# Kernel tuning notes

Measured on AMD Instinct MI355X. Metric: run time of the kernel, lower is better.

The kernel has to match this reference:

```python
import jax, jax.numpy as jnp
import numpy as np

TEMPERATURE = 0.5
NEG_INF = -1e9  # used to mask self-similarity diagonal before logsumexp


def setup_inputs() -> dict:
    key = jax.random.key(0)
    k1, k2 = jax.random.split(key)
    N, Z = 4096, 128
    z1 = jax.random.normal(k1, (N, Z), dtype=jnp.float32)
    z2 = jax.random.normal(k2, (N, Z), dtype=jnp.float32)
    return {"z1": z1, "z2": z2}


def reference(z1, z2):
    # NT-Xent (SimCLR) loss. Faithful to:
    #   sim = cosine_similarity over all pairs of concat([z1, z2])
    #   positives = sim diagonals at offsets +-N; negatives = all off-(self)diag entries
    #   cross_entropy with the positive as class 0  ->  -pos/T + logsumexp(all non-self sims / T)
    N = z1.shape[0]
    reps = jnp.concatenate([z1, z2], axis=0)                      # [2N, Z]
    # row-normalize once; cosine sim matrix is then a single GEMM
    norms = jnp.linalg.norm(reps, axis=-1, keepdims=True)
    # torch cosine_similarity clamps norms by eps=1e-8
    nreps = reps / jnp.maximum(norms, 1e-8)
    sim = nreps @ nreps.T                                          # [2N, 2N]
    # positives: sim[i, i+N] for i<N and sim[i, i-N] for i>=N
    l_pos = jnp.diagonal(sim, offset=N)                            # [N]
    r_pos = jnp.diagonal(sim, offset=-N)                           # [N]
    positives = jnp.concatenate([l_pos, r_pos])                    # [2N]
    # logsumexp over all entries except the self-similarity diagonal.
    # (The positive entry stays in the denominator exactly once, matching
    #  concat([positive, negatives]) in the original.)
    two_n = 2 * N
    self_mask = jnp.eye(two_n, dtype=bool)
    logits = jnp.where(self_mask, NEG_INF, sim / TEMPERATURE)      # [2N, 2N]
    lse = jax.nn.logsumexp(logits, axis=1)                         # [2N]
    per_row = lse - positives / TEMPERATURE                        # CE with label 0
    return jnp.sum(per_row) / two_n
```

## Files before the change

kernel.cpp:

```cpp
#include <hip/hip_runtime.h>
#include <hip/hip_bf16.h>


#define N_PAIRS 4096
#define ZDIM    128
#define NROWS   8192
#define QS 1.6986437717f

typedef __bf16 bf16x8 __attribute__((ext_vector_type(8)));
typedef float  floatx4 __attribute__((ext_vector_type(4)));

__global__ __launch_bounds__(256) void k_normalize(
    const float* __restrict__ z1, const float* __restrict__ z2,
    __hip_bfloat16* __restrict__ pack, float* __restrict__ pos,
    float* __restrict__ denom)
{
    const int zi = blockIdx.x * 256 + threadIdx.x;
    if (zi < NROWS) denom[zi] = 0.0f;

    const int w = threadIdx.x >> 6;
    const int lane = threadIdx.x & 63;
    const int p = blockIdx.x * 4 + w;
    const float2 a = ((const float2*)(z1 + (size_t)p * ZDIM))[lane];
    const float2 b = ((const float2*)(z2 + (size_t)p * ZDIM))[lane];
    float s1 = a.x * a.x + a.y * a.y;
    float s2 = b.x * b.x + b.y * b.y;
    float d  = a.x * b.x + a.y * b.y;
    #pragma unroll
    for (int off = 1; off < 64; off <<= 1) {
        s1 += __shfl_xor(s1, off, 64);
        s2 += __shfl_xor(s2, off, 64);
        d  += __shfl_xor(d,  off, 64);
    }
    const float n1 = fmaxf(sqrtf(s1), 1e-8f);
    const float n2 = fmaxf(sqrtf(s2), 1e-8f);
    const float i1 = 1.0f / n1, i2 = 1.0f / n2;
    const float q1 = i1 * QS, q2 = i2 * QS;
    float2 na; na.x = a.x * q1; na.y = a.y * q1;
    float2 nb; nb.x = b.x * q2; nb.y = b.y * q2;

    const int ks = lane >> 4;
    const int qq = (lane >> 2) & 3;
    const int jj = (lane & 3) * 2;
    const int r1 = p, r2 = p + N_PAIRS;
    const size_t i1e = ((size_t)((r1 >> 4) * 4 + ks)) * 512 + qq * 128 + (r1 & 15) * 8 + jj;
    const size_t i2e = ((size_t)((r2 >> 4) * 4 + ks)) * 512 + qq * 128 + (r2 & 15) * 8 + jj;
    *(__hip_bfloat162*)(pack + i1e) = __float22bfloat162_rn(na);
    *(__hip_bfloat162*)(pack + i2e) = __float22bfloat162_rn(nb);
    if (lane == 0) pos[p] = d * i1 * i2;
}

__global__ __launch_bounds__(256) void k_simsum(
    const __hip_bfloat16* __restrict__ pack, float* __restrict__ denom)
{
    const int tid  = threadIdx.x;
    const int lane = tid & 63;
    const int w    = tid >> 6;
    const int rt   = blockIdx.x >> 4;
    const int cs   = blockIdx.x & 15;
    const int q    = lane >> 4;
    const int l16  = lane & 15;

    const int rowb = rt * 128 + w * 32;
    const __hip_bfloat16* Abase =
        pack + ((size_t)(rowb >> 4) * 4) * 512 + lane * 8;
    bf16x8 afrag[2][4];
    #pragma unroll
    for (int mt = 0; mt < 2; ++mt)
        #pragma unroll
        for (int ks = 0; ks < 4; ++ks)
            afrag[mt][ks] = *(const bf16x8*)(Abase + mt * 2048 + ks * 512);

    float rowsum[2][4];
    #pragma unroll
    for (int mt = 0; mt < 2; ++mt)
        #pragma unroll
        for (int r = 0; r < 4; ++r) rowsum[mt][r] = 0.0f;

    for (int it = 0; it < 8; ++it) {
        floatx4 acc[2][4];
        #pragma unroll
        for (int mt = 0; mt < 2; ++mt)
            #pragma unroll
            for (int nt = 0; nt < 4; ++nt) {
                acc[mt][nt].x = 0.f; acc[mt][nt].y = 0.f;
                acc[mt][nt].z = 0.f; acc[mt][nt].w = 0.f;
            }
        const int colb = cs * 512 + it * 64;
        const __hip_bfloat16* Bbase =
            pack + ((size_t)(colb >> 4) * 4) * 512 + lane * 8;
        bf16x8 bfrag[4][4];
        #pragma unroll
        for (int nt = 0; nt < 4; ++nt)
            #pragma unroll
            for (int ks = 0; ks < 4; ++ks)
                bfrag[nt][ks] = *(const bf16x8*)(Bbase + nt * 2048 + ks * 512);
        #pragma unroll
        for (int ks = 0; ks < 4; ++ks)
            #pragma unroll
            for (int mt = 0; mt < 2; ++mt)
                #pragma unroll
                for (int nt = 0; nt < 4; ++nt)
                    acc[mt][nt] = __builtin_amdgcn_mfma_f32_16x16x32_bf16(
                        afrag[mt][ks], bfrag[nt][ks], acc[mt][nt], 0, 0, 0);
        #pragma unroll
        for (int mt = 0; mt < 2; ++mt) {
            const int rowtb = rowb + mt * 16;
            #pragma unroll
            for (int nt = 0; nt < 4; ++nt) {
                const int coltb = colb + nt * 16;
                if (rowtb == coltb) {
                    #pragma unroll
                    for (int r = 0; r < 4; ++r) {
                        const float e = __builtin_amdgcn_exp2f(acc[mt][nt][r]);
                        rowsum[mt][r] += (l16 == q * 4 + r) ? 0.0f : e;
                    }
                } else {
                    #pragma unroll
                    for (int r = 0; r < 4; ++r)
                        rowsum[mt][r] += __builtin_amdgcn_exp2f(acc[mt][nt][r]);
                }
            }
        }
    }

    #pragma unroll
    for (int mt = 0; mt < 2; ++mt)
        #pragma unroll
        for (int r = 0; r < 4; ++r) {
            float s = rowsum[mt][r];
            s += __shfl_xor(s, 1, 64);
            s += __shfl_xor(s, 2, 64);
            s += __shfl_xor(s, 4, 64);
            s += __shfl_xor(s, 8, 64);
            rowsum[mt][r] = s;
        }
    if (l16 == 0) {
        #pragma unroll
        for (int mt = 0; mt < 2; ++mt)
            #pragma unroll
            for (int r = 0; r < 4; ++r) {
                const int grow = rowb + mt * 16 + q * 4 + r;
                atomicAdd(&denom[grow], rowsum[mt][r]);
            }
    }
}

__global__ __launch_bounds__(1024) void k_finish(
    const float* __restrict__ denom, const float* __restrict__ pos,
    float* __restrict__ out)
{
    __shared__ float red[1024];
    const int t = threadIdx.x;
    float s = 0.0f;
    for (int i = t; i < NROWS; i += 1024) s += __logf(denom[i]);
    float p = 0.0f;
    for (int i = t; i < N_PAIRS; i += 1024) p += pos[i];
    red[t] = s - 4.0f * p;
    __syncthreads();
    for (int off = 512; off > 0; off >>= 1) {
        if (t < off) red[t] += red[t + off];
        __syncthreads();
    }
    if (t == 0) out[0] = red[0] / (float)NROWS;
}

extern "C" void kernel_launch(void* const* d_in, const int* in_sizes, int n_in,
                              void* d_out, int out_size, void* d_ws, size_t ws_size,
                              hipStream_t stream) {
    const float* z1 = (const float*)d_in[0];
    const float* z2 = (const float*)d_in[1];
    float* out = (float*)d_out;

    char* ws = (char*)d_ws;
    __hip_bfloat16* pack = (__hip_bfloat16*)ws;
    float* denom = (float*)(ws + (size_t)NROWS * ZDIM * 2);
    float* pos   = denom + NROWS;

    k_normalize<<<N_PAIRS / 4, 256, 0, stream>>>(z1, z2, pack, pos, denom);
    k_simsum<<<1024, 256, 0, stream>>>(pack, denom);
    k_finish<<<1, 1024, 0, stream>>>(denom, pos, out);
}
```

Before: 87.64 us.

## Exploit similarity matrix symmetry by computing only upper-triangular tiles

```diff
diff --git a/kernel.cpp b/kernel.cpp
--- a/kernel.cpp
+++ b/kernel.cpp
@@ -53,11 +53,14 @@
 __global__ __launch_bounds__(256) void k_simsum(
     const __hip_bfloat16* __restrict__ pack, float* __restrict__ denom)
 {
+    const int rt = blockIdx.x;
+    const int ct = blockIdx.y;
+    if (ct < rt) return;
+    const bool diag = (rt == ct);
+
     const int tid  = threadIdx.x;
     const int lane = tid & 63;
     const int w    = tid >> 6;
-    const int rt   = blockIdx.x >> 4;
-    const int cs   = blockIdx.x & 15;
     const int q    = lane >> 4;
     const int l16  = lane & 15;
 
@@ -72,12 +75,14 @@
             afrag[mt][ks] = *(const bf16x8*)(Abase + mt * 2048 + ks * 512);
 
     float rowsum[2][4];
-    #pragma unroll
-    for (int mt = 0; mt < 2; ++mt)
-        #pragma unroll
-        for (int r = 0; r < 4; ++r) rowsum[mt][r] = 0.0f;
-
-    for (int it = 0; it < 8; ++it) {
+    float colsum[2][4];
+    #pragma unroll
+    for (int a = 0; a < 2; ++a)
+        #pragma unroll
+        for (int b = 0; b < 4; ++b) { rowsum[a][b] = 0.0f; colsum[a][b] = 0.0f; }
+
+    #pragma unroll
+    for (int it = 0; it < 2; ++it) {
         floatx4 acc[2][4];
         #pragma unroll
         for (int mt = 0; mt < 2; ++mt)
@@ -86,7 +91,7 @@
                 acc[mt][nt].x = 0.f; acc[mt][nt].y = 0.f;
                 acc[mt][nt].z = 0.f; acc[mt][nt].w = 0.f;
             }
-        const int colb = cs * 512 + it * 64;
+        const int colb = ct * 128 + it * 64;
         const __hip_bfloat16* Bbase =
             pack + ((size_t)(colb >> 4) * 4) * 512 + lane * 8;
         bf16x8 bfrag[4][4];
@@ -103,24 +108,38 @@
                 for (int nt = 0; nt < 4; ++nt)
                     acc[mt][nt] = __builtin_amdgcn_mfma_f32_16x16x32_bf16(
                         afrag[mt][ks], bfrag[nt][ks], acc[mt][nt], 0, 0, 0);
-        #pragma unroll
-        for (int mt = 0; mt < 2; ++mt) {
-            const int rowtb = rowb + mt * 16;
-            #pragma unroll
-            for (int nt = 0; nt < 4; ++nt) {
-                const int coltb = colb + nt * 16;
-                if (rowtb == coltb) {
+
+        if (diag) {
+            #pragma unroll
+            for (int mt = 0; mt < 2; ++mt) {
+                const int rowtb = w * 32 + mt * 16;
+                #pragma unroll
+                for (int nt = 0; nt < 4; ++nt) {
+                    const int coltb = it * 64 + nt * 16;
+                    if (rowtb == coltb) {
+                        #pragma unroll
+                        for (int r = 0; r < 4; ++r) {
+                            const float e = __builtin_amdgcn_exp2f(acc[mt][nt][r]);
+                            rowsum[mt][r] += (l16 == q * 4 + r) ? 0.0f : e;
+                        }
+                    } else {
+                        #pragma unroll
+                        for (int r = 0; r < 4; ++r)
+                            rowsum[mt][r] += __builtin_amdgcn_exp2f(acc[mt][nt][r]);
+                    }
+                }
+            }
+        } else {
+            #pragma unroll
+            for (int mt = 0; mt < 2; ++mt)
+                #pragma unroll
+                for (int nt = 0; nt < 4; ++nt)
                     #pragma unroll
                     for (int r = 0; r < 4; ++r) {
                         const float e = __builtin_amdgcn_exp2f(acc[mt][nt][r]);
-                        rowsum[mt][r] += (l16 == q * 4 + r) ? 0.0f : e;
+                        rowsum[mt][r] += e;
+                        colsum[it][nt] += e;
                     }
-                } else {
-                    #pragma unroll
-                    for (int r = 0; r < 4; ++r)
-                        rowsum[mt][r] += __builtin_amdgcn_exp2f(acc[mt][nt][r]);
-                }
-            }
         }
     }
 
@@ -144,25 +163,42 @@
                 atomicAdd(&denom[grow], rowsum[mt][r]);
             }
     }
+    if (!diag) {
+        #pragma unroll
+        for (int it = 0; it < 2; ++it)
+            #pragma unroll
+            for (int nt = 0; nt < 4; ++nt) {
+                float s = colsum[it][nt];
+                s += __shfl_xor(s, 16, 64);
+                s += __shfl_xor(s, 32, 64);
+                if (q == 0)
+                    atomicAdd(&denom[ct * 128 + it * 64 + nt * 16 + l16], s);
+            }
+    }
 }
 
 __global__ __launch_bounds__(1024) void k_finish(
     const float* __restrict__ denom, const float* __restrict__ pos,
     float* __restrict__ out)
 {
-    __shared__ float red[1024];
+    __shared__ float red[16];
     const int t = threadIdx.x;
+    const int lane = t & 63, wv = t >> 6;
     float s = 0.0f;
     for (int i = t; i < NROWS; i += 1024) s += __logf(denom[i]);
     float p = 0.0f;
     for (int i = t; i < N_PAIRS; i += 1024) p += pos[i];
-    red[t] = s - 4.0f * p;
+    float v = s - 4.0f * p;
+    #pragma unroll
+    for (int off = 1; off < 64; off <<= 1) v += __shfl_xor(v, off, 64);
+    if (lane == 0) red[wv] = v;
     __syncthreads();
-    for (int off = 512; off > 0; off >>= 1) {
-        if (t < off) red[t] += red[t + off];
-        __syncthreads();
-    }
-    if (t == 0) out[0] = red[0] / (float)NROWS;
+    if (wv == 0) {
+        float x = (lane < 16) ? red[lane] : 0.0f;
+        #pragma unroll
+        for (int off = 1; off < 16; off <<= 1) x += __shfl_xor(x, off, 64);
+        if (lane == 0) out[0] = x / (float)NROWS;
+    }
 }
 
 extern "C" void kernel_launch(void* const* d_in, const int* in_sizes, int n_in,
@@ -178,6 +214,6 @@
     float* pos   = denom + NROWS;
 
     k_normalize<<<N_PAIRS / 4, 256, 0, stream>>>(z1, z2, pack, pos, denom);
-    k_simsum<<<1024, 256, 0, stream>>>(pack, denom);
+    k_simsum<<<dim3(64, 64), 256, 0, stream>>>(pack, denom);
     k_finish<<<1, 1024, 0, stream>>>(denom, pos, out);
 }
```

Measured after the change: 94.97 us. 8.4% more time.

## Enlarge per-wave row tile and double-buffer B fragments in similarity kernel

Applied to the files above, without the earlier changes.

```diff
diff --git a/kernel.cpp b/kernel.cpp
--- a/kernel.cpp
+++ b/kernel.cpp
@@ -61,53 +61,57 @@
     const int q    = lane >> 4;
     const int l16  = lane & 15;
 
-    const int rowb = rt * 128 + w * 32;
+    const int rowb = rt * 256 + w * 64;
     const __hip_bfloat16* Abase =
         pack + ((size_t)(rowb >> 4) * 4) * 512 + lane * 8;
-    bf16x8 afrag[2][4];
-    #pragma unroll
-    for (int mt = 0; mt < 2; ++mt)
+    bf16x8 afrag[4][4];
+    #pragma unroll
+    for (int mt = 0; mt < 4; ++mt)
         #pragma unroll
         for (int ks = 0; ks < 4; ++ks)
             afrag[mt][ks] = *(const bf16x8*)(Abase + mt * 2048 + ks * 512);
 
-    float rowsum[2][4];
-    #pragma unroll
-    for (int mt = 0; mt < 2; ++mt)
+    float rowsum[4][4];
+    #pragma unroll
+    for (int mt = 0; mt < 4; ++mt)
         #pragma unroll
         for (int r = 0; r < 4; ++r) rowsum[mt][r] = 0.0f;
 
-    for (int it = 0; it < 8; ++it) {
-        floatx4 acc[2][4];
-        #pragma unroll
-        for (int mt = 0; mt < 2; ++mt)
-            #pragma unroll
-            for (int nt = 0; nt < 4; ++nt) {
+    const __hip_bfloat16* Bcol0 =
+        pack + ((size_t)((cs * 512) >> 4) * 4) * 512 + lane * 8;
+
+    auto loadB = [&](bf16x8 (&buf)[4][2], int hs) {
+        const __hip_bfloat16* bp = Bcol0 + (size_t)hs * 4096;
+        #pragma unroll
+        for (int ks = 0; ks < 4; ++ks)
+            #pragma unroll
+            for (int nt = 0; nt < 2; ++nt)
+                buf[ks][nt] = *(const bf16x8*)(bp + nt * 2048 + ks * 512);
+    };
+
+    auto compute = [&](bf16x8 (&buf)[4][2], int hs) {
+        floatx4 acc[4][2];
+        #pragma unroll
+        for (int mt = 0; mt < 4; ++mt)
+            #pragma unroll
+            for (int nt = 0; nt < 2; ++nt) {
                 acc[mt][nt].x = 0.f; acc[mt][nt].y = 0.f;
                 acc[mt][nt].z = 0.f; acc[mt][nt].w = 0.f;
             }
-        const int colb = cs * 512 + it * 64;
-        const __hip_bfloat16* Bbase =
-            pack + ((size_t)(colb >> 4) * 4) * 512 + lane * 8;
-        bf16x8 bfrag[4][4];
-        #pragma unroll
-        for (int nt = 0; nt < 4; ++nt)
-            #pragma unroll
-            for (int ks = 0; ks < 4; ++ks)
-                bfrag[nt][ks] = *(const bf16x8*)(Bbase + nt * 2048 + ks * 512);
         #pragma unroll
         for (int ks = 0; ks < 4; ++ks)
             #pragma unroll
-            for (int mt = 0; mt < 2; ++mt)
+            for (int mt = 0; mt < 4; ++mt)
                 #pragma unroll
-                for (int nt = 0; nt < 4; ++nt)
+                for (int nt = 0; nt < 2; ++nt)
                     acc[mt][nt] = __builtin_amdgcn_mfma_f32_16x16x32_bf16(
-                        afrag[mt][ks], bfrag[nt][ks], acc[mt][nt], 0, 0, 0);
-        #pragma unroll
-        for (int mt = 0; mt < 2; ++mt) {
+                        afrag[mt][ks], buf[ks][nt], acc[mt][nt], 0, 0, 0);
+        const int colb = cs * 512 + hs * 32;
+        #pragma unroll
+        for (int mt = 0; mt < 4; ++mt) {
             const int rowtb = rowb + mt * 16;
             #pragma unroll
-            for (int nt = 0; nt < 4; ++nt) {
+            for (int nt = 0; nt < 2; ++nt) {
                 const int coltb = colb + nt * 16;
                 if (rowtb == coltb) {
                     #pragma unroll
@@ -122,10 +126,19 @@
                 }
             }
         }
-    }
-
-    #pragma unroll
-    for (int mt = 0; mt < 2; ++mt)
+    };
+
+    bf16x8 bufA[4][2], bufB[4][2];
+    loadB(bufA, 0);
+    for (int hs = 0; hs < 16; hs += 2) {
+        loadB(bufB, hs + 1);
+        compute(bufA, hs);
+        loadB(bufA, (hs + 2) & 15);
+        compute(bufB, hs + 1);
+    }
+
+    #pragma unroll
+    for (int mt = 0; mt < 4; ++mt)
         #pragma unroll
         for (int r = 0; r < 4; ++r) {
             float s = rowsum[mt][r];
@@ -137,7 +150,7 @@
         }
     if (l16 == 0) {
         #pragma unroll
-        for (int mt = 0; mt < 2; ++mt)
+        for (int mt = 0; mt < 4; ++mt)
             #pragma unroll
             for (int r = 0; r < 4; ++r) {
                 const int grow = rowb + mt * 16 + q * 4 + r;
@@ -150,19 +163,24 @@
     const float* __restrict__ denom, const float* __restrict__ pos,
     float* __restrict__ out)
 {
-    __shared__ float red[1024];
+    __shared__ float red[16];
     const int t = threadIdx.x;
+    const int lane = t & 63, wv = t >> 6;
     float s = 0.0f;
     for (int i = t; i < NROWS; i += 1024) s += __logf(denom[i]);
     float p = 0.0f;
     for (int i = t; i < N_PAIRS; i += 1024) p += pos[i];
-    red[t] = s - 4.0f * p;
+    float v = s - 4.0f * p;
+    #pragma unroll
+    for (int off = 1; off < 64; off <<= 1) v += __shfl_xor(v, off, 64);
+    if (lane == 0) red[wv] = v;
     __syncthreads();
-    for (int off = 512; off > 0; off >>= 1) {
-        if (t < off) red[t] += red[t + off];
-        __syncthreads();
-    }
-    if (t == 0) out[0] = red[0] / (float)NROWS;
+    if (wv == 0) {
+        float x = (lane < 16) ? red[lane] : 0.0f;
+        #pragma unroll
+        for (int off = 1; off < 16; off <<= 1) x += __shfl_xor(x, off, 64);
+        if (lane == 0) out[0] = x / (float)NROWS;
+    }
 }
 
 extern "C" void kernel_launch(void* const* d_in, const int* in_sizes, int n_in,
@@ -178,6 +196,6 @@
     float* pos   = denom + NROWS;
 
     k_normalize<<<N_PAIRS / 4, 256, 0, stream>>>(z1, z2, pack, pos, denom);
-    k_simsum<<<1024, 256, 0, stream>>>(pack, denom);
+    k_simsum<<<512, 256, 0, stream>>>(pack, denom);
     k_finish<<<1, 1024, 0, stream>>>(denom, pos, out);
 }
```

Result: faster. 83.40 us (-4.8%).
